# Kernel tuning notes

Hardware: AMD Instinct MI355X
Metric: run time of the kernel (lower is better)

## Reference

```python
import jax, jax.numpy as jnp
import numpy as np

N_NODES = 100000
N_EDGES = 3200000
ALPHA_KCL = 1.0
ALPHA_KVL = 1.0
EPS = 1e-6


def setup_inputs() -> dict:
    key = jax.random.key(0)
    k1, k2, k3, k4 = jax.random.split(key, 4)
    node_features = jax.random.normal(k1, (N_NODES, 4), dtype=jnp.float32)
    edge_index = jax.random.randint(k2, (2, N_EDGES), 0, N_NODES, dtype=jnp.int64)
    edge_logits = jax.random.normal(k3, (N_EDGES,), dtype=jnp.float32)
    edge_params = jax.random.uniform(k4, (N_EDGES, 2), dtype=jnp.float32)
    return {
        "node_features": node_features,
        "edge_index": edge_index,
        "edge_logits": edge_logits,
        "edge_params": edge_params,
    }


def reference(node_features, edge_index, edge_logits, edge_params):
    n_nodes = node_features.shape[0]
    edge_probs = jax.nn.sigmoid(edge_logits)  # [E]
    src = edge_index[0]  # [E]
    dst = edge_index[1]  # [E]
    v = node_features[:, 0]  # [N] voltage column
    # per-edge current: |v_src - v_dst| / (R + X + eps) * prob
    v_diff = jnp.abs(v[src] - v[dst])
    impedance = edge_params[:, 0] + edge_params[:, 1]
    current = v_diff / (impedance + EPS) * edge_probs  # [E]
    # KCL: each edge subtracts its current at src, adds at dst
    node_sum = (
        jax.ops.segment_sum(current, dst, num_segments=n_nodes)
        - jax.ops.segment_sum(current, src, num_segments=n_nodes)
    )  # [N]
    kcl_loss = jnp.mean(node_sum ** 2)
    # KVL (simplified): mean of per-column unbiased variance of edge_params
    kvl_loss = jnp.var(edge_params, axis=0, ddof=1).mean()
    return ALPHA_KCL * kcl_loss + ALPHA_KVL * kvl_loss
```

## Files before the change

kernel.cpp:

```cpp
#include <hip/hip_runtime.h>
#include <math.h>

#define N_NODES 100000
#define N_EDGES 3200000
#define EPS_F 1e-6f
#define PAIRS   (N_EDGES / 2)

#define TBL_N   80000
#define GNB     256
#define GSTRIDE (GNB * 1024)
#define NVARW   (GNB * 16)

#define SLICE_N 12500
#define NSLICE  8
#define NCHUNK  32
#define C_PAIRS (PAIRS / NCHUNK)
#define SBATCH  8

#define NKCLB   391
#define NPACKB  196

#define CNT_WORD  32
#define PK_OFF    64
#define PART_OFF  (PK_OFF + 2 * N_EDGES)
#define VARP_OFF  (PART_OFF + NCHUNK * N_NODES)
#define KCLP_OFF  (VARP_OFF + 4 * NVARW)
#define VBF_OFF   (KCLP_OFF + 512)
#define WS_FLOATS (VBF_OFF + N_NODES / 2 + 64)

__device__ __forceinline__ float wave_reduce(float v) {
    #pragma unroll
    for (int off = 32; off > 0; off >>= 1) v += __shfl_down(v, off, 64);
    return v;
}

__device__ __forceinline__ void fadd_agent(float* p, float v) {
    unsafeAtomicAdd(p, v);
}

__device__ __forceinline__ unsigned short f2bf(float f) {
    unsigned u = __float_as_uint(f);
    unsigned r = ((u >> 16) & 1u) + 0x7FFFu;
    return (unsigned short)((u + r) >> 16);
}
__device__ __forceinline__ float bf2f(unsigned short h) {
    return __uint_as_float(((unsigned)h) << 16);
}

__global__ __launch_bounds__(256) void pack_kernel(
    const float* __restrict__ nf, float* __restrict__ ws)
{
    const int t = blockIdx.x * 256 + threadIdx.x;
    if (t == 0) ((unsigned*)ws)[CNT_WORD] = 0;
    if (t < N_NODES / 2) {
        const float4 a = ((const float4*)nf)[2 * t];
        const float4 b = ((const float4*)nf)[2 * t + 1];
        ((unsigned*)(ws + VBF_OFF))[t] = (unsigned)f2bf(a.x) | ((unsigned)f2bf(b.x) << 16);
    }
}

__global__ __launch_bounds__(1024, 4) void prep_kernel(
    const void*   __restrict__ eidx,
    const float*  __restrict__ logits,
    const float2* __restrict__ params,
    float*        __restrict__ ws)
{
    __shared__ unsigned vlds[TBL_N / 2];

    const unsigned* vsrc = (const unsigned*)(ws + VBF_OFF);
    for (int j = threadIdx.x; j < TBL_N / 2; j += 1024) vlds[j] = vsrc[j];

    const int* i32 = (const int*)eidx;
    int any = 0;
    #pragma unroll
    for (int k = 1; k < 32; k += 2) any |= i32[k];
    const bool is32 = (any != 0);

    __syncthreads();
    const unsigned short* vl = (const unsigned short*)vlds;
    const unsigned short* vg = (const unsigned short*)(ws + VBF_OFF);

    const int gtid = blockIdx.x * 1024 + threadIdx.x;
    int4* pk = (int4*)(ws + PK_OFF);

    float s0 = 0.f, s1 = 0.f, q0 = 0.f, q1 = 0.f;

    #define VGET(id) bf2f(((unsigned)(id) < TBL_N) ? vl[id] : vg[id])

    for (int p = gtid; p < PAIRS; p += 4 * GSTRIDE) {
        int pi[4];
        #pragma unroll
        for (int u = 0; u < 4; ++u) {
            const int pp = p + u * GSTRIDE;
            pi[u] = (pp < PAIRS) ? pp : p;
        }

        int2 sp[4], dp[4];
        if (is32) {
            #pragma unroll
            for (int u = 0; u < 4; ++u) {
                sp[u] = ((const int2*)i32)[pi[u]];
                dp[u] = ((const int2*)(i32 + N_EDGES))[pi[u]];
            }
        } else {
            #pragma unroll
            for (int u = 0; u < 4; ++u) {
                const int4 a = ((const int4*)i32)[pi[u]];
                const int4 b = ((const int4*)(i32 + 2 * N_EDGES))[pi[u]];
                sp[u] = make_int2(a.x, a.z);
                dp[u] = make_int2(b.x, b.z);
            }
        }

        float4 ppr[4];
        float2 lgr[4];
        #pragma unroll
        for (int u = 0; u < 4; ++u) {
            ppr[u] = ((const float4*)params)[pi[u]];
            lgr[u] = ((const float2*)logits)[pi[u]];
        }

        float vs0[4], vd0[4], vs1[4], vd1[4];
        #pragma unroll
        for (int u = 0; u < 4; ++u) {
            vs0[u] = VGET(sp[u].x);  vd0[u] = VGET(dp[u].x);
            vs1[u] = VGET(sp[u].y);  vd1[u] = VGET(dp[u].y);
        }

        #pragma unroll
        for (int u = 0; u < 4; ++u) {
            const int pp = p + u * GSTRIDE;
            const float w0 = (1.0f / (1.0f + __expf(-lgr[u].x))) / (ppr[u].x + ppr[u].y + EPS_F);
            const float w1 = (1.0f / (1.0f + __expf(-lgr[u].y))) / (ppr[u].z + ppr[u].w + EPS_F);
            const float c0 = fabsf(vs0[u] - vd0[u]) * w0;
            const float c1 = fabsf(vs1[u] - vd1[u]) * w1;

            int4 o;
            o.x = (int)((unsigned)sp[u].x | ((unsigned)dp[u].x << 17));
            o.y = (int)((((unsigned)dp[u].x) >> 15) | ((unsigned)f2bf(c0) << 2));
            o.z = (int)((unsigned)sp[u].y | ((unsigned)dp[u].y << 17));
            o.w = (int)((((unsigned)dp[u].y) >> 15) | ((unsigned)f2bf(c1) << 2));

            if (pp < PAIRS) {
                pk[pp] = o;
                s0 += ppr[u].x + ppr[u].z;
                s1 += ppr[u].y + ppr[u].w;
                q0 += ppr[u].x * ppr[u].x + ppr[u].z * ppr[u].z;
                q1 += ppr[u].y * ppr[u].y + ppr[u].w * ppr[u].w;
            }
        }
    }
    #undef VGET

    s0 = wave_reduce(s0); s1 = wave_reduce(s1);
    q0 = wave_reduce(q0); q1 = wave_reduce(q1);

    if ((threadIdx.x & 63) == 0) {
        float4 o; o.x = s0; o.y = s1; o.z = q0; o.w = q1;
        ((float4*)(ws + VARP_OFF))[blockIdx.x * 16 + (threadIdx.x >> 6)] = o;
    }
}

__global__ __launch_bounds__(1024) void scatter_kernel(float* __restrict__ ws)
{
    __shared__ float bins[SLICE_N];

    const int c  = blockIdx.x & (NCHUNK - 1);
    const int s  = blockIdx.x >> 5;
    const unsigned lo = (unsigned)(s * SLICE_N);

    for (int j = threadIdx.x; j < SLICE_N; j += 1024) bins[j] = 0.f;
    __syncthreads();

    const int4* pk = (const int4*)(ws + PK_OFF);

    const int p0 = c * C_PAIRS;
    const int p1 = p0 + C_PAIRS;

    for (int base = p0 + (int)threadIdx.x; base < p1; base += 1024 * SBATCH) {
        int4 q[SBATCH];
        #pragma unroll
        for (int k = 0; k < SBATCH; ++k) {
            int p = base + k * 1024;
            p = (p < p1) ? p : (p1 - 1);
            q[k] = pk[p];
        }
        #pragma unroll
        for (int k = 0; k < SBATCH; ++k) {
            const int p = base + k * 1024;
            if (p < p1) {
                const unsigned lo0 = (unsigned)q[k].x, hi0 = (unsigned)q[k].y;
                const unsigned lo1 = (unsigned)q[k].z, hi1 = (unsigned)q[k].w;
                const unsigned s0 = (lo0 & 0x1FFFFu) - lo;
                const unsigned d0 = ((lo0 >> 17) | ((hi0 & 3u) << 15)) - lo;
                const unsigned s1 = (lo1 & 0x1FFFFu) - lo;
                const unsigned d1 = ((lo1 >> 17) | ((hi1 & 3u) << 15)) - lo;
                const float c0 = bf2f((unsigned short)((hi0 >> 2) & 0xFFFFu));
                const float c1 = bf2f((unsigned short)((hi1 >> 2) & 0xFFFFu));
                if (d0 < SLICE_N) atomicAdd(&bins[d0],  c0);
                if (s0 < SLICE_N) atomicAdd(&bins[s0], -c0);
                if (d1 < SLICE_N) atomicAdd(&bins[d1],  c1);
                if (s1 < SLICE_N) atomicAdd(&bins[s1], -c1);
            }
        }
    }
    __syncthreads();

    float4* pt4 = (float4*)(ws + PART_OFF + (size_t)c * N_NODES + lo);
    for (int j = threadIdx.x; j < SLICE_N / 4; j += 1024)
        pt4[j] = ((const float4*)bins)[j];
}

__global__ __launch_bounds__(256) void kclfinal_kernel(float* __restrict__ ws,
                                                       float* __restrict__ out)
{
    __shared__ float red[4];
    __shared__ unsigned last;

    const int i = blockIdx.x * blockDim.x + threadIdx.x;
    float acc = 0.f;
    if (i < N_NODES) {
        const float* p = ws + PART_OFF + i;
        float s = 0.f;
        #pragma unroll 8
        for (int c = 0; c < NCHUNK; ++c) s += p[(size_t)c * N_NODES];
        acc = s * s;
    }
    acc = wave_reduce(acc);
    if ((threadIdx.x & 63) == 0) red[threadIdx.x >> 6] = acc;
    __syncthreads();
    if (threadIdx.x == 0) {
        ws[KCLP_OFF + blockIdx.x] = red[0] + red[1] + red[2] + red[3];
        __threadfence();
        const unsigned old = atomicAdd((unsigned*)ws + CNT_WORD, 1u);
        last = (old == NKCLB - 1) ? 1u : 0u;
    }
    __syncthreads();
    if (!last) return;

    __shared__ float red2[4][5];
    float s0 = 0.f, s1 = 0.f, q0 = 0.f, q1 = 0.f, k = 0.f;

    const float4* vp = (const float4*)(ws + VARP_OFF);
    for (int j = threadIdx.x; j < NVARW; j += 256) {
        const float4 v = vp[j];
        s0 += v.x; s1 += v.y; q0 += v.z; q1 += v.w;
    }
    for (int j = threadIdx.x; j < NKCLB; j += 256)
        k += unsafeAtomicAdd(ws + KCLP_OFF + j, 0.0f);

    s0 = wave_reduce(s0); s1 = wave_reduce(s1);
    q0 = wave_reduce(q0); q1 = wave_reduce(q1);
    k  = wave_reduce(k);

    const int wid = threadIdx.x >> 6;
    if ((threadIdx.x & 63) == 0) {
        red2[wid][0] = s0; red2[wid][1] = s1; red2[wid][2] = q0;
        red2[wid][3] = q1; red2[wid][4] = k;
    }
    __syncthreads();
    if (threadIdx.x == 0) {
        float a0 = 0.f, a1 = 0.f, a2 = 0.f, a3 = 0.f, a4 = 0.f;
        #pragma unroll
        for (int w = 0; w < 4; ++w) {
            a0 += red2[w][0]; a1 += red2[w][1]; a2 += red2[w][2];
            a3 += red2[w][3]; a4 += red2[w][4];
        }
        const float n    = (float)N_EDGES;
        const float var0 = (a2 - a0 * a0 / n) / (n - 1.0f);
        const float var1 = (a3 - a1 * a1 / n) / (n - 1.0f);
        out[0] = a4 / (float)N_NODES + 0.5f * (var0 + var1);
    }
}

#define FB_NODE_OFF 64
__global__ __launch_bounds__(256) void edge_kernel_fb(
    const float*  __restrict__ nf,
    const void*   __restrict__ eidx,
    const float*  __restrict__ logits,
    const float2* __restrict__ params,
    float*        __restrict__ ws)
{
    const int*       i32 = (const int*)eidx;
    const long long* i64 = (const long long*)eidx;
    int any = 0;
    #pragma unroll
    for (int k = 1; k < 32; k += 2) any |= i32[k];
    const bool is32 = (any != 0);

    float* node_sum = ws + FB_NODE_OFF;
    float* acc      = ws + 1;

    float s0 = 0.f, s1 = 0.f, q0 = 0.f, q1 = 0.f;
    const int tid    = blockIdx.x * blockDim.x + threadIdx.x;
    const int stride = gridDim.x * blockDim.x;
    for (int i = tid; i < N_EDGES; i += stride) {
        int src, dst;
        if (is32) { src = i32[i]; dst = i32[N_EDGES + i]; }
        else      { src = (int)i64[i]; dst = (int)i64[N_EDGES + i]; }
        const float2 ep = params[i];
        const float  p  = 1.0f / (1.0f + __expf(-logits[i]));
        const float cur = fabsf(nf[src * 4] - nf[dst * 4]) / (ep.x + ep.y + EPS_F) * p;
        fadd_agent(node_sum + dst,  cur);
        fadd_agent(node_sum + src, -cur);
        s0 += ep.x; s1 += ep.y; q0 += ep.x * ep.x; q1 += ep.y * ep.y;
    }
    s0 = wave_reduce(s0); s1 = wave_reduce(s1);
    q0 = wave_reduce(q0); q1 = wave_reduce(q1);
    if ((threadIdx.x & 63) == 0) {
        fadd_agent(acc + 0, s0); fadd_agent(acc + 1, s1);
        fadd_agent(acc + 2, q0); fadd_agent(acc + 3, q1);
    }
}

__global__ __launch_bounds__(256) void kcl_kernel_fb(float* __restrict__ ws)
{
    const float* node_sum = ws + FB_NODE_OFF;
    float acc = 0.f;
    const int tid    = blockIdx.x * blockDim.x + threadIdx.x;
    const int stride = gridDim.x * blockDim.x;
    for (int i = tid; i < N_NODES; i += stride) {
        const float v = node_sum[i];
        acc += v * v;
    }
    acc = wave_reduce(acc);
    if ((threadIdx.x & 63) == 0) fadd_agent(ws + 5, acc);
}

__global__ void final_kernel_fb(const float* __restrict__ ws, float* __restrict__ out)
{
    const float s0 = ws[1], s1 = ws[2], q0 = ws[3], q1 = ws[4], k = ws[5];
    const float n  = (float)N_EDGES;
    const float var0 = (q0 - s0 * s0 / n) / (n - 1.0f);
    const float var1 = (q1 - s1 * s1 / n) / (n - 1.0f);
    out[0] = k / (float)N_NODES + 0.5f * (var0 + var1);
}

extern "C" void kernel_launch(void* const* d_in, const int* in_sizes, int n_in,
                              void* d_out, int out_size, void* d_ws, size_t ws_size,
                              hipStream_t stream) {
    const float*  nf     = (const float*)d_in[0];
    const void*   eidx   = d_in[1];
    const float*  logits = (const float*)d_in[2];
    const float2* params = (const float2*)d_in[3];
    float* ws  = (float*)d_ws;
    float* out = (float*)d_out;

    const size_t need = (size_t)WS_FLOATS * sizeof(float);

    if (ws_size >= need) {
        pack_kernel<<<NPACKB, 256, 0, stream>>>(nf, ws);
        prep_kernel<<<GNB, 1024, 0, stream>>>(eidx, logits, params, ws);
        scatter_kernel<<<NCHUNK * NSLICE, 1024, 0, stream>>>(ws);
        kclfinal_kernel<<<NKCLB, 256, 0, stream>>>(ws, out);
    } else {
        hipMemsetAsync(d_ws, 0, 256 + (size_t)N_NODES * sizeof(float), stream);
        edge_kernel_fb<<<2048, 256, 0, stream>>>(nf, eidx, logits, params, ws);
        kcl_kernel_fb<<<200, 256, 0, stream>>>(ws);
        final_kernel_fb<<<1, 1, 0, stream>>>(ws, out);
    }
}
```

Measured before the change: 168.6 us.

## Fuse pack, prep, scatter and reduction into one cooperative kernel with grid syncs

Merges the four separate launches (bf16 voltage pack, edge prep, sliced scatter, KCL/KVL final reduction) into a single cooperative kernel of 256 blocks that separates the phases with grid.sync. Shared memory is unioned across phases. The aim is to remove per-launch overhead and the idle gaps between kernels. In exchange it adds grid-wide barrier costs, and the final reduction now runs on a single block. If the cooperative launch fails, it falls back to the old multi-kernel path.

```diff
diff --git a/kernel.cpp b/kernel.cpp
--- a/kernel.cpp
+++ b/kernel.cpp
@@ -1,5 +1,8 @@
 #include <hip/hip_runtime.h>
+#include <hip/hip_cooperative_groups.h>
 #include <math.h>
+
+namespace cg = cooperative_groups;
 
 #define N_NODES 100000
 #define N_EDGES 3200000
@@ -47,6 +50,233 @@
     return __uint_as_float(((unsigned)h) << 16);
 }
 
+__global__ __launch_bounds__(1024, 4) void fused_kernel(
+    const float*  __restrict__ nf,
+    const void*   __restrict__ eidx,
+    const float*  __restrict__ logits,
+    const float2* __restrict__ params,
+    float*        __restrict__ ws,
+    float*        __restrict__ out)
+{
+    cg::grid_group grid = cg::this_grid();
+
+    __shared__ union {
+        unsigned table[TBL_N / 2];
+        float    bins[SLICE_N];
+        float    sc[16];
+        float    red2[16][5];
+    } u;
+
+    const int t  = threadIdx.x;
+    const int b  = blockIdx.x;
+    const int gt = b * 1024 + t;
+
+    if (gt < N_NODES / 2) {
+        const float4 a = ((const float4*)nf)[2 * gt];
+        const float4 c = ((const float4*)nf)[2 * gt + 1];
+        ((unsigned*)(ws + VBF_OFF))[gt] = (unsigned)f2bf(a.x) | ((unsigned)f2bf(c.x) << 16);
+    }
+    grid.sync();
+
+    {
+        const unsigned* vsrc = (const unsigned*)(ws + VBF_OFF);
+        for (int j = t; j < TBL_N / 2; j += 1024) u.table[j] = vsrc[j];
+
+        const int* i32 = (const int*)eidx;
+        int any = 0;
+        #pragma unroll
+        for (int k = 1; k < 32; k += 2) any |= i32[k];
+        const bool is32 = (any != 0);
+
+        __syncthreads();
+        const unsigned short* vl = (const unsigned short*)u.table;
+        const unsigned short* vg = (const unsigned short*)(ws + VBF_OFF);
+
+        int4* pk = (int4*)(ws + PK_OFF);
+        float s0 = 0.f, s1 = 0.f, q0 = 0.f, q1 = 0.f;
+
+        #define VGET(id) bf2f(((unsigned)(id) < TBL_N) ? vl[id] : vg[id])
+
+        for (int p = gt; p < PAIRS; p += 4 * GSTRIDE) {
+            int pi[4];
+            #pragma unroll
+            for (int uu = 0; uu < 4; ++uu) {
+                const int pp = p + uu * GSTRIDE;
+                pi[uu] = (pp < PAIRS) ? pp : p;
+            }
+
+            int2 sp[4], dp[4];
+            if (is32) {
+                #pragma unroll
+                for (int uu = 0; uu < 4; ++uu) {
+                    sp[uu] = ((const int2*)i32)[pi[uu]];
+                    dp[uu] = ((const int2*)(i32 + N_EDGES))[pi[uu]];
+                }
+            } else {
+                #pragma unroll
+                for (int uu = 0; uu < 4; ++uu) {
+                    const int4 a = ((const int4*)i32)[pi[uu]];
+                    const int4 c = ((const int4*)(i32 + 2 * N_EDGES))[pi[uu]];
+                    sp[uu] = make_int2(a.x, a.z);
+                    dp[uu] = make_int2(c.x, c.z);
+                }
+            }
+
+            float4 ppr[4];
+            float2 lgr[4];
+            #pragma unroll
+            for (int uu = 0; uu < 4; ++uu) {
+                ppr[uu] = ((const float4*)params)[pi[uu]];
+                lgr[uu] = ((const float2*)logits)[pi[uu]];
+            }
+
+            float vs0[4], vd0[4], vs1[4], vd1[4];
+            #pragma unroll
+            for (int uu = 0; uu < 4; ++uu) {
+                vs0[uu] = VGET(sp[uu].x);  vd0[uu] = VGET(dp[uu].x);
+                vs1[uu] = VGET(sp[uu].y);  vd1[uu] = VGET(dp[uu].y);
+            }
+
+            #pragma unroll
+            for (int uu = 0; uu < 4; ++uu) {
+                const int pp = p + uu * GSTRIDE;
+                const float w0 = (1.0f / (1.0f + __expf(-lgr[uu].x))) / (ppr[uu].x + ppr[uu].y + EPS_F);
+                const float w1 = (1.0f / (1.0f + __expf(-lgr[uu].y))) / (ppr[uu].z + ppr[uu].w + EPS_F);
+                const float c0 = fabsf(vs0[uu] - vd0[uu]) * w0;
+                const float c1 = fabsf(vs1[uu] - vd1[uu]) * w1;
+
+                int4 o;
+                o.x = (int)((unsigned)sp[uu].x | ((unsigned)dp[uu].x << 17));
+                o.y = (int)((((unsigned)dp[uu].x) >> 15) | ((unsigned)f2bf(c0) << 2));
+                o.z = (int)((unsigned)sp[uu].y | ((unsigned)dp[uu].y << 17));
+                o.w = (int)((((unsigned)dp[uu].y) >> 15) | ((unsigned)f2bf(c1) << 2));
+
+                if (pp < PAIRS) {
+                    pk[pp] = o;
+                    s0 += ppr[uu].x + ppr[uu].z;
+                    s1 += ppr[uu].y + ppr[uu].w;
+                    q0 += ppr[uu].x * ppr[uu].x + ppr[uu].z * ppr[uu].z;
+                    q1 += ppr[uu].y * ppr[uu].y + ppr[uu].w * ppr[uu].w;
+                }
+            }
+        }
+        #undef VGET
+
+        s0 = wave_reduce(s0); s1 = wave_reduce(s1);
+        q0 = wave_reduce(q0); q1 = wave_reduce(q1);
+        if ((t & 63) == 0) {
+            float4 o; o.x = s0; o.y = s1; o.z = q0; o.w = q1;
+            ((float4*)(ws + VARP_OFF))[b * 16 + (t >> 6)] = o;
+        }
+    }
+    grid.sync();
+
+    {
+        const int c  = b & (NCHUNK - 1);
+        const int s  = b >> 5;
+        const unsigned lo = (unsigned)(s * SLICE_N);
+
+        for (int j = t; j < SLICE_N; j += 1024) u.bins[j] = 0.f;
+        __syncthreads();
+
+        const int4* pk = (const int4*)(ws + PK_OFF);
+        const int p0 = c * C_PAIRS;
+        const int p1 = p0 + C_PAIRS;
+
+        for (int base = p0 + t; base < p1; base += 1024 * SBATCH) {
+            int4 q[SBATCH];
+            #pragma unroll
+            for (int k = 0; k < SBATCH; ++k) {
+                int p = base + k * 1024;
+                p = (p < p1) ? p : (p1 - 1);
+                q[k] = pk[p];
+            }
+            #pragma unroll
+            for (int k = 0; k < SBATCH; ++k) {
+                const int p = base + k * 1024;
+                if (p < p1) {
+                    const unsigned lo0 = (unsigned)q[k].x, hi0 = (unsigned)q[k].y;
+                    const unsigned lo1 = (unsigned)q[k].z, hi1 = (unsigned)q[k].w;
+                    const unsigned s0 = (lo0 & 0x1FFFFu) - lo;
+                    const unsigned d0 = ((lo0 >> 17) | ((hi0 & 3u) << 15)) - lo;
+                    const unsigned s1 = (lo1 & 0x1FFFFu) - lo;
+                    const unsigned d1 = ((lo1 >> 17) | ((hi1 & 3u) << 15)) - lo;
+                    const float c0 = bf2f((unsigned short)((hi0 >> 2) & 0xFFFFu));
+                    const float c1 = bf2f((unsigned short)((hi1 >> 2) & 0xFFFFu));
+                    if (d0 < SLICE_N) atomicAdd(&u.bins[d0],  c0);
+                    if (s0 < SLICE_N) atomicAdd(&u.bins[s0], -c0);
+                    if (d1 < SLICE_N) atomicAdd(&u.bins[d1],  c1);
+                    if (s1 < SLICE_N) atomicAdd(&u.bins[s1], -c1);
+                }
+            }
+        }
+        __syncthreads();
+
+        float4* pt4 = (float4*)(ws + PART_OFF + (size_t)c * N_NODES + lo);
+        for (int j = t; j < SLICE_N / 4; j += 1024)
+            pt4[j] = ((const float4*)u.bins)[j];
+    }
+    grid.sync();
+
+    {
+        float acc = 0.f;
+        if (gt < N_NODES) {
+            const float* p = ws + PART_OFF + gt;
+            float s = 0.f;
+            #pragma unroll 8
+            for (int c = 0; c < NCHUNK; ++c) s += p[(size_t)c * N_NODES];
+            acc = s * s;
+        }
+        acc = wave_reduce(acc);
+        __syncthreads();
+        if ((t & 63) == 0) u.sc[t >> 6] = acc;
+        __syncthreads();
+        if (t == 0) {
+            float s = 0.f;
+            #pragma unroll
+            for (int w = 0; w < 16; ++w) s += u.sc[w];
+            ws[KCLP_OFF + b] = s;
+        }
+    }
+    grid.sync();
+
+    if (b == 0) {
+        float s0 = 0.f, s1 = 0.f, q0 = 0.f, q1 = 0.f, k = 0.f;
+
+        const float4* vp = (const float4*)(ws + VARP_OFF);
+        for (int j = t; j < NVARW; j += 1024) {
+            const float4 v = vp[j];
+            s0 += v.x; s1 += v.y; q0 += v.z; q1 += v.w;
+        }
+        for (int j = t; j < GNB; j += 1024) k += ws[KCLP_OFF + j];
+
+        s0 = wave_reduce(s0); s1 = wave_reduce(s1);
+        q0 = wave_reduce(q0); q1 = wave_reduce(q1);
+        k  = wave_reduce(k);
+
+        __syncthreads();
+        const int wid = t >> 6;
+        if ((t & 63) == 0) {
+            u.red2[wid][0] = s0; u.red2[wid][1] = s1; u.red2[wid][2] = q0;
+            u.red2[wid][3] = q1; u.red2[wid][4] = k;
+        }
+        __syncthreads();
+        if (t == 0) {
+            float a0 = 0.f, a1 = 0.f, a2 = 0.f, a3 = 0.f, a4 = 0.f;
+            #pragma unroll
+            for (int w = 0; w < 16; ++w) {
+                a0 += u.red2[w][0]; a1 += u.red2[w][1]; a2 += u.red2[w][2];
+                a3 += u.red2[w][3]; a4 += u.red2[w][4];
+            }
+            const float n    = (float)N_EDGES;
+            const float var0 = (a2 - a0 * a0 / n) / (n - 1.0f);
+            const float var1 = (a3 - a1 * a1 / n) / (n - 1.0f);
+            out[0] = a4 / (float)N_NODES + 0.5f * (var0 + var1);
+        }
+    }
+}
+
+
 __global__ __launch_bounds__(256) void pack_kernel(
     const float* __restrict__ nf, float* __restrict__ ws)
 {
@@ -82,11 +312,9 @@
 
     const int gtid = blockIdx.x * 1024 + threadIdx.x;
     int4* pk = (int4*)(ws + PK_OFF);
-
     float s0 = 0.f, s1 = 0.f, q0 = 0.f, q1 = 0.f;
 
     #define VGET(id) bf2f(((unsigned)(id) < TBL_N) ? vl[id] : vg[id])
-
     for (int p = gtid; p < PAIRS; p += 4 * GSTRIDE) {
         int pi[4];
         #pragma unroll
@@ -94,7 +322,6 @@
             const int pp = p + u * GSTRIDE;
             pi[u] = (pp < PAIRS) ? pp : p;
         }
-
         int2 sp[4], dp[4];
         if (is32) {
             #pragma unroll
@@ -111,7 +338,6 @@
                 dp[u] = make_int2(b.x, b.z);
             }
         }
-
         float4 ppr[4];
         float2 lgr[4];
         #pragma unroll
@@ -119,14 +345,12 @@
             ppr[u] = ((const float4*)params)[pi[u]];
             lgr[u] = ((const float2*)logits)[pi[u]];
         }
-
         float vs0[4], vd0[4], vs1[4], vd1[4];
         #pragma unroll
         for (int u = 0; u < 4; ++u) {
             vs0[u] = VGET(sp[u].x);  vd0[u] = VGET(dp[u].x);
             vs1[u] = VGET(sp[u].y);  vd1[u] = VGET(dp[u].y);
         }
-
         #pragma unroll
         for (int u = 0; u < 4; ++u) {
             const int pp = p + u * GSTRIDE;
@@ -134,13 +358,11 @@
             const float w1 = (1.0f / (1.0f + __expf(-lgr[u].y))) / (ppr[u].z + ppr[u].w + EPS_F);
             const float c0 = fabsf(vs0[u] - vd0[u]) * w0;
             const float c1 = fabsf(vs1[u] - vd1[u]) * w1;
-
             int4 o;
             o.x = (int)((unsigned)sp[u].x | ((unsigned)dp[u].x << 17));
             o.y = (int)((((unsigned)dp[u].x) >> 15) | ((unsigned)f2bf(c0) << 2));
             o.z = (int)((unsigned)sp[u].y | ((unsigned)dp[u].y << 17));
             o.w = (int)((((unsigned)dp[u].y) >> 15) | ((unsigned)f2bf(c1) << 2));
-
             if (pp < PAIRS) {
                 pk[pp] = o;
                 s0 += ppr[u].x + ppr[u].z;
@@ -154,7 +376,6 @@
 
     s0 = wave_reduce(s0); s1 = wave_reduce(s1);
     q0 = wave_reduce(q0); q1 = wave_reduce(q1);
-
     if ((threadIdx.x & 63) == 0) {
         float4 o; o.x = s0; o.y = s1; o.z = q0; o.w = q1;
         ((float4*)(ws + VARP_OFF))[blockIdx.x * 16 + (threadIdx.x >> 6)] = o;
@@ -173,7 +394,6 @@
     __syncthreads();
 
     const int4* pk = (const int4*)(ws + PK_OFF);
-
     const int p0 = c * C_PAIRS;
     const int p1 = p0 + C_PAIRS;
 
@@ -349,10 +569,19 @@
     const size_t need = (size_t)WS_FLOATS * sizeof(float);
 
     if (ws_size >= need) {
-        pack_kernel<<<NPACKB, 256, 0, stream>>>(nf, ws);
-        prep_kernel<<<GNB, 1024, 0, stream>>>(eidx, logits, params, ws);
-        scatter_kernel<<<NCHUNK * NSLICE, 1024, 0, stream>>>(ws);
-        kclfinal_kernel<<<NKCLB, 256, 0, stream>>>(ws, out);
+        void* kargs[6];
+        kargs[0] = (void*)&nf;     kargs[1] = (void*)&eidx;
+        kargs[2] = (void*)&logits; kargs[3] = (void*)&params;
+        kargs[4] = (void*)&ws;     kargs[5] = (void*)&out;
+        const hipError_t e = hipLaunchCooperativeKernel(
+            (const void*)fused_kernel, dim3(GNB), dim3(1024), kargs, 0, stream);
+        if (e != hipSuccess) {
+            (void)hipGetLastError();
+            pack_kernel<<<NPACKB, 256, 0, stream>>>(nf, ws);
+            prep_kernel<<<GNB, 1024, 0, stream>>>(eidx, logits, params, ws);
+            scatter_kernel<<<NCHUNK * NSLICE, 1024, 0, stream>>>(ws);
+            kclfinal_kernel<<<NKCLB, 256, 0, stream>>>(ws, out);
+        }
     } else {
         hipMemsetAsync(d_ws, 0, 256 + (size_t)N_NODES * sizeof(float), stream);
         edge_kernel_fb<<<2048, 256, 0, stream>>>(nf, eidx, logits, params, ws);
```

Result: slower. 299.7 us (+77.8%).
